# Kernel optimization log

Hardware: AMD Instinct MI355X
Metric: run time of the kernel (lower is better)

Reference implementation:

```python
import jax, jax.numpy as jnp
import numpy as np
import math

HIDDEN = 2048
N_HEADS = 32
N_KV_HEADS = 8
HEAD_DIM = HIDDEN // N_HEADS  # 64
N_REP = N_HEADS // N_KV_HEADS  # 4
ROPE_THETA = 10000.0
BSZ, SEQ = 2, 2048


def setup_inputs() -> dict:
    key = jax.random.key(0)
    ks = jax.random.split(key, 6)
    hidden_states = jax.random.normal(ks[0], (BSZ, SEQ, HIDDEN), dtype=jnp.float32)
    wq = jax.random.normal(ks[1], (HIDDEN, N_HEADS * HEAD_DIM), dtype=jnp.float32) * (HIDDEN ** -0.5)
    wk = jax.random.normal(ks[2], (HIDDEN, N_KV_HEADS * HEAD_DIM), dtype=jnp.float32) * (HIDDEN ** -0.5)
    wv = jax.random.normal(ks[3], (HIDDEN, N_KV_HEADS * HEAD_DIM), dtype=jnp.float32) * (HIDDEN ** -0.5)
    wo = jax.random.normal(ks[4], (N_HEADS * HEAD_DIM, HIDDEN), dtype=jnp.float32) * (HIDDEN ** -0.5)
    # additive causal mask [b, 1, q, kv]
    neg = jnp.finfo(jnp.float32).min
    causal = jnp.where(jnp.tril(jnp.ones((SEQ, SEQ), dtype=bool)), 0.0, neg)
    attention_mask = jnp.broadcast_to(causal[None, None], (BSZ, 1, SEQ, SEQ)).astype(jnp.float32)
    position_ids = jnp.broadcast_to(jnp.arange(SEQ, dtype=jnp.int32)[None], (BSZ, SEQ))
    return {
        "hidden_states": hidden_states,
        "wq": wq, "wk": wk, "wv": wv, "wo": wo,
        "attention_mask": attention_mask,
        "position_ids": position_ids,
    }


def _rope_cache(seq_len, dtype):
    inv_freq = 1.0 / (ROPE_THETA ** (jnp.arange(0, HEAD_DIM, 2, dtype=jnp.float32) / HEAD_DIM))
    t = jnp.arange(seq_len, dtype=jnp.float32)
    freqs = jnp.outer(t, inv_freq)              # [S, head_dim/2]
    emb = jnp.concatenate([freqs, freqs], -1)   # [S, head_dim]
    return jnp.cos(emb).astype(dtype), jnp.sin(emb).astype(dtype)


def _rotate_half(x):
    x1, x2 = jnp.split(x, 2, axis=-1)
    return jnp.concatenate([-x2, x1], axis=-1)


def reference(hidden_states, wq, wk, wv, wo, attention_mask, position_ids):
    b, s, _ = hidden_states.shape
    q = (hidden_states @ wq).reshape(b, s, N_HEADS, HEAD_DIM).transpose(0, 2, 1, 3)
    k = (hidden_states @ wk).reshape(b, s, N_KV_HEADS, HEAD_DIM).transpose(0, 2, 1, 3)
    v = (hidden_states @ wv).reshape(b, s, N_KV_HEADS, HEAD_DIM).transpose(0, 2, 1, 3)

    cos_c, sin_c = _rope_cache(s, hidden_states.dtype)
    cos = cos_c[position_ids][:, None]  # [b,1,s,head_dim]
    sin = sin_c[position_ids][:, None]
    q = q * cos + _rotate_half(q) * sin
    k = k * cos + _rotate_half(k) * sin

    # repeat_kv: [b, kvh, s, d] -> [b, kvh*n_rep, s, d]
    k = jnp.broadcast_to(k[:, :, None], (b, N_KV_HEADS, N_REP, s, HEAD_DIM)).reshape(b, N_HEADS, s, HEAD_DIM)
    v = jnp.broadcast_to(v[:, :, None], (b, N_KV_HEADS, N_REP, s, HEAD_DIM)).reshape(b, N_HEADS, s, HEAD_DIM)

    scores = jnp.einsum('bhqd,bhkd->bhqk', q, k) / math.sqrt(HEAD_DIM)
    scores = scores + attention_mask
    probs = jax.nn.softmax(scores.astype(jnp.float32), axis=-1).astype(q.dtype)
    attn = jnp.einsum('bhqk,bhkd->bhqd', probs, v)  # [b,h,s,d]
    attn = attn.transpose(0, 2, 1, 3).reshape(b, s, N_HEADS * HEAD_DIM)
    return attn @ wo
```

## Files before the change

kernel.cpp:

```cpp
#include <hip/hip_runtime.h>
#include <math.h>


typedef float f32x4 __attribute__((ext_vector_type(4)));
typedef short s16x8 __attribute__((ext_vector_type(8)));
typedef unsigned short u16x4 __attribute__((ext_vector_type(4)));

__device__ __forceinline__ unsigned short f2bf(float x) {
    union { float f; unsigned int u; } v; v.f = x;
    unsigned int r = v.u + 0x7FFF + ((v.u >> 16) & 1);
    return (unsigned short)(r >> 16);
}

__global__ __launch_bounds__(256) void cast_f32_bf16(
    const float* __restrict__ in, unsigned short* __restrict__ out) {
    size_t i = (size_t)blockIdx.x * 256 + threadIdx.x;
    f32x4 v = *(const f32x4*)&in[i * 4];
    u16x4 r;
    r[0] = f2bf(v[0]); r[1] = f2bf(v[1]); r[2] = f2bf(v[2]); r[3] = f2bf(v[3]);
    *(u16x4*)&out[i * 4] = r;
}

__global__ __launch_bounds__(256) void transpose_cast_all(
    const float* __restrict__ Wq, const float* __restrict__ Wk,
    const float* __restrict__ Wv, const float* __restrict__ Wo,
    unsigned short* __restrict__ Wqkvt, unsigned short* __restrict__ Wot) {
    __shared__ float t[32][33];
    const int bx = blockIdx.x;
    const float* W; unsigned short* Out; int N, n0, nb;
    if (bx < 64)      { W = Wq; Out = Wqkvt; N = 2048; n0 = 0;    nb = bx; }
    else if (bx < 80) { W = Wk; Out = Wqkvt; N = 512;  n0 = 2048; nb = bx - 64; }
    else if (bx < 96) { W = Wv; Out = Wqkvt; N = 512;  n0 = 2560; nb = bx - 80; }
    else              { W = Wo; Out = Wot;   N = 2048; n0 = 0;    nb = bx - 96; }
    int kb = blockIdx.y * 32; nb *= 32;
    int tx = threadIdx.x & 31, ty = threadIdx.x >> 5;
#pragma unroll
    for (int i = 0; i < 4; ++i)
        t[ty + i * 8][tx] = W[(size_t)(kb + ty + i * 8) * N + nb + tx];
    __syncthreads();
#pragma unroll
    for (int i = 0; i < 4; ++i)
        Out[(size_t)(n0 + nb + ty + i * 8) * 2048 + kb + tx] = f2bf(t[tx][ty + i * 8]);
}

__global__ __launch_bounds__(256) void gemm_qkv_rope(
    const unsigned short* __restrict__ A, const unsigned short* __restrict__ Bt,
    const int* __restrict__ pos,
    unsigned short* __restrict__ Qb, unsigned short* __restrict__ Kb,
    unsigned short* __restrict__ Vb) {
    const int K = 2048;
    __shared__ unsigned short As[128 * 64];
    __shared__ unsigned short Bs[128 * 64];
    const int tid = threadIdx.x;
    const int wave = tid >> 6, lane = tid & 63;
    const int col = lane & 15, quad = lane >> 4;
    const int m0 = blockIdx.y * 128, n0 = blockIdx.x * 128;
    const int wm = (wave >> 1) * 64, wn = (wave & 1) * 64;

    const int lrow = lane >> 3;
    const int gch = (lane & 7) ^ lrow;
    const unsigned short* Ag = A + (size_t)(m0 + wave * 32 + lrow) * K + gch * 8;
    const unsigned short* Bg = Bt + (size_t)(n0 + wave * 32 + lrow) * K + gch * 8;
    unsigned short* AsW = As + wave * 2048;
    unsigned short* BsW = Bs + wave * 2048;

    f32x4 acc[4][4] = {};

    for (int k0 = 0; k0 < K; k0 += 64) {
#pragma unroll
        for (int i = 0; i < 4; ++i) {
            __builtin_amdgcn_global_load_lds(
                (const __attribute__((address_space(1))) void*)(Ag + (size_t)i * 8 * K + k0),
                (__attribute__((address_space(3))) void*)(AsW + i * 512), 16, 0, 0);
            __builtin_amdgcn_global_load_lds(
                (const __attribute__((address_space(1))) void*)(Bg + (size_t)i * 8 * K + k0),
                (__attribute__((address_space(3))) void*)(BsW + i * 512), 16, 0, 0);
        }
        __syncthreads();
#pragma unroll
        for (int ks = 0; ks < 2; ++ks) {
            const int slot = ((ks << 2) + quad) ^ (col & 7);
            s16x8 af[4], bf[4];
#pragma unroll
            for (int mi = 0; mi < 4; ++mi)
                af[mi] = *(const s16x8*)&As[(wm + mi * 16 + col) * 64 + slot * 8];
#pragma unroll
            for (int ni = 0; ni < 4; ++ni)
                bf[ni] = *(const s16x8*)&Bs[(wn + ni * 16 + col) * 64 + slot * 8];
#pragma unroll
            for (int mi = 0; mi < 4; ++mi)
#pragma unroll
                for (int ni = 0; ni < 4; ++ni)
                    acc[mi][ni] = __builtin_amdgcn_mfma_f32_16x16x32_bf16(
                        af[mi], bf[ni], acc[mi][ni], 0, 0, 0);
        }
        __syncthreads();
    }

    const int cb = n0 + wn;
    if (cb >= 2560) {
        const int hd = (cb - 2560) >> 6;
#pragma unroll
        for (int mi = 0; mi < 4; ++mi)
#pragma unroll
            for (int r = 0; r < 4; ++r) {
                int m = m0 + wm + mi * 16 + quad * 4 + r;
                int b = m >> 11, s = m & 2047;
                size_t rb = ((size_t)(b * 8 + hd) * 2048 + s) * 64;
#pragma unroll
                for (int ni = 0; ni < 4; ++ni)
                    Vb[rb + ni * 16 + col] = f2bf(acc[mi][ni][r]);
            }
    } else {
        const int isQ = (cb < 2048);
        const int hd = isQ ? (cb >> 6) : ((cb - 2048) >> 6);
        const int nh = isQ ? 32 : 8;
        const float scale = isQ ? 0.125f : 1.0f;
        unsigned short* Out = isQ ? Qb : Kb;
        const float NEG_LN_TH_32 = -0.28782313662425575f;
        const float inv0 = __expf((float)col * NEG_LN_TH_32);
        const float inv1 = __expf((float)(col + 16) * NEG_LN_TH_32);
#pragma unroll
        for (int mi = 0; mi < 4; ++mi)
#pragma unroll
            for (int r = 0; r < 4; ++r) {
                int m = m0 + wm + mi * 16 + quad * 4 + r;
                int b = m >> 11, s = m & 2047;
                float p = (float)pos[m];
                float sn0, cs0, sn1, cs1;
                __sincosf(p * inv0, &sn0, &cs0);
                __sincosf(p * inv1, &sn1, &cs1);
                float a0 = acc[mi][0][r], a1 = acc[mi][1][r];
                float b0 = acc[mi][2][r], b1 = acc[mi][3][r];
                size_t rb = ((size_t)(b * nh + hd) * 2048 + s) * 64;
                Out[rb + col]      = f2bf((a0 * cs0 - b0 * sn0) * scale);
                Out[rb + col + 16] = f2bf((a1 * cs1 - b1 * sn1) * scale);
                Out[rb + col + 32] = f2bf((b0 * cs0 + a0 * sn0) * scale);
                Out[rb + col + 48] = f2bf((b1 * cs1 + a1 * sn1) * scale);
            }
    }
}

__global__ __launch_bounds__(256) void gemm_bf16_nt(
    const unsigned short* __restrict__ A, const unsigned short* __restrict__ Bt,
    float* __restrict__ C, int K, int ldc) {
    __shared__ unsigned short As[128 * 64];
    __shared__ unsigned short Bs[128 * 64];
    const int tid = threadIdx.x;
    const int wave = tid >> 6, lane = tid & 63;
    const int col = lane & 15, quad = lane >> 4;
    const int m0 = blockIdx.y * 128, n0 = blockIdx.x * 128;
    const int wm = (wave >> 1) * 64, wn = (wave & 1) * 64;

    const int lrow = lane >> 3;
    const int gch = (lane & 7) ^ lrow;
    const unsigned short* Ag = A + (size_t)(m0 + wave * 32 + lrow) * K + gch * 8;
    const unsigned short* Bg = Bt + (size_t)(n0 + wave * 32 + lrow) * K + gch * 8;
    unsigned short* AsW = As + wave * 2048;
    unsigned short* BsW = Bs + wave * 2048;

    f32x4 acc[4][4] = {};

    for (int k0 = 0; k0 < K; k0 += 64) {
#pragma unroll
        for (int i = 0; i < 4; ++i) {
            __builtin_amdgcn_global_load_lds(
                (const __attribute__((address_space(1))) void*)(Ag + (size_t)i * 8 * K + k0),
                (__attribute__((address_space(3))) void*)(AsW + i * 512), 16, 0, 0);
            __builtin_amdgcn_global_load_lds(
                (const __attribute__((address_space(1))) void*)(Bg + (size_t)i * 8 * K + k0),
                (__attribute__((address_space(3))) void*)(BsW + i * 512), 16, 0, 0);
        }
        __syncthreads();
#pragma unroll
        for (int ks = 0; ks < 2; ++ks) {
            const int slot = ((ks << 2) + quad) ^ (col & 7);
            s16x8 af[4], bf[4];
#pragma unroll
            for (int mi = 0; mi < 4; ++mi)
                af[mi] = *(const s16x8*)&As[(wm + mi * 16 + col) * 64 + slot * 8];
#pragma unroll
            for (int ni = 0; ni < 4; ++ni)
                bf[ni] = *(const s16x8*)&Bs[(wn + ni * 16 + col) * 64 + slot * 8];
#pragma unroll
            for (int mi = 0; mi < 4; ++mi)
#pragma unroll
                for (int ni = 0; ni < 4; ++ni)
                    acc[mi][ni] = __builtin_amdgcn_mfma_f32_16x16x32_bf16(
                        af[mi], bf[ni], acc[mi][ni], 0, 0, 0);
        }
        __syncthreads();
    }
#pragma unroll
    for (int mi = 0; mi < 4; ++mi)
#pragma unroll
        for (int ni = 0; ni < 4; ++ni)
#pragma unroll
            for (int r = 0; r < 4; ++r) {
                int m = m0 + wm + mi * 16 + quad * 4 + r;
                int n = n0 + wn + ni * 16 + col;
                C[(size_t)m * ldc + n] = acc[mi][ni][r];
            }
}

__global__ __launch_bounds__(256) void transpose_v(
    const unsigned short* __restrict__ Vb, unsigned short* __restrict__ Vt) {
    __shared__ unsigned short t[64 * 66];
    const int bh = blockIdx.x >> 5, st = blockIdx.x & 31;
    const unsigned short* src = Vb + ((size_t)bh * 2048 + st * 64) * 64;
    unsigned short* dst = Vt + (size_t)bh * 64 * 2048 + st * 64;
    const int r = threadIdx.x >> 2, c = (threadIdx.x & 3) * 16;
    s16x8 v0 = *(const s16x8*)&src[r * 64 + c];
    s16x8 v1 = *(const s16x8*)&src[r * 64 + c + 8];
    unsigned* tw = (unsigned*)&t[r * 66 + c];
#pragma unroll
    for (int q2 = 0; q2 < 4; ++q2) tw[q2] = ((unsigned*)&v0)[q2];
#pragma unroll
    for (int q2 = 0; q2 < 4; ++q2) tw[4 + q2] = ((unsigned*)&v1)[q2];
    __syncthreads();
    const int d = threadIdx.x >> 2, sc2 = (threadIdx.x & 3) * 16;
    unsigned short outv[16];
#pragma unroll
    for (int jj = 0; jj < 16; ++jj) outv[jj] = t[(sc2 + jj) * 66 + d];
    *(s16x8*)&dst[(size_t)d * 2048 + sc2] = *(s16x8*)&outv[0];
    *(s16x8*)&dst[(size_t)d * 2048 + sc2 + 8] = *(s16x8*)&outv[8];
}

__global__ __launch_bounds__(256, 4) void flash_attn(
    const unsigned short* __restrict__ Qb, const unsigned short* __restrict__ Kb,
    const unsigned short* __restrict__ Vt, unsigned short* __restrict__ Ob) {
    __shared__ unsigned short Ks[64 * 64];
    __shared__ unsigned short Vs[64 * 64];
    __shared__ unsigned short PsA[4][16 * 64];
    __shared__ unsigned short PsB[4][16 * 64];

    const int tid = threadIdx.x;
    const int wave = tid >> 6, lane = tid & 63;
    const int col = lane & 15, quad = lane >> 4;

    const int id = blockIdx.x;
    const int j = id & 15, bh = id >> 4;
    const int b = bh >> 5, h = bh & 31, kvh = h >> 2;
    const int qA0 = (31 - j) * 64, qB0 = j * 64;
    const int qwA = qA0 + wave * 16, qwB = qB0 + wave * 16;

    const unsigned short* Qg  = Qb + ((size_t)(b * 32 + h) * 2048) * 64;
    const unsigned short* Kgb = Kb + ((size_t)(b * 8 + kvh) * 2048) * 64;
    const unsigned short* Vgb = Vt + ((size_t)(b * 8 + kvh) * 64) * 2048;

    const int r8 = lane >> 3, g = (lane & 7) ^ r8;
    const unsigned short* KgL = Kgb + (size_t)(wave * 16 + r8) * 64 + g * 8;
    const unsigned short* VgL = Vgb + (size_t)(wave * 16 + r8) * 2048 + g * 8;
    unsigned short* KsW = Ks + wave * 16 * 64;
    unsigned short* VsW = Vs + wave * 16 * 64;

    const s16x8 onesf = {16256, 16256, 16256, 16256, 16256, 16256, 16256, 16256};

    s16x8 qfA[2], qfB[2];
#pragma unroll
    for (int ks = 0; ks < 2; ++ks) {
        qfA[ks] = *(const s16x8*)&Qg[(size_t)(qwA + col) * 64 + ks * 32 + quad * 8];
        qfB[ks] = *(const s16x8*)&Qg[(size_t)(qwB + col) * 64 + ks * 32 + quad * 8];
    }

    f32x4 aoA[4] = {}, aoB[4] = {};
    f32x4 alA = {}, alB = {};

    for (int kv0 = 0; kv0 <= qA0; kv0 += 64) {
        __builtin_amdgcn_global_load_lds(
            (const __attribute__((address_space(1))) void*)(KgL + (size_t)kv0 * 64),
            (__attribute__((address_space(3))) void*)KsW, 16, 0, 0);
        __builtin_amdgcn_global_load_lds(
            (const __attribute__((address_space(1))) void*)(KgL + (size_t)kv0 * 64 + 512),
            (__attribute__((address_space(3))) void*)(KsW + 512), 16, 0, 0);
        __builtin_amdgcn_global_load_lds(
            (const __attribute__((address_space(1))) void*)(VgL + kv0),
            (__attribute__((address_space(3))) void*)VsW, 16, 0, 0);
        __builtin_amdgcn_global_load_lds(
            (const __attribute__((address_space(1))) void*)(VgL + kv0 + 8 * 2048),
            (__attribute__((address_space(3))) void*)(VsW + 512), 16, 0, 0);
        __syncthreads();

        const bool doB = (kv0 <= qB0);
#pragma unroll
        for (int mi = 0; mi < 4; ++mi) {
            const int s0 = (quad) ^ (col & 7);
            const int s1 = (4 + quad) ^ (col & 7);
            s16x8 kf0 = *(const s16x8*)&Ks[(mi * 16 + col) * 64 + s0 * 8];
            s16x8 kf1 = *(const s16x8*)&Ks[(mi * 16 + col) * 64 + s1 * 8];
            {
                f32x4 sc = {};
                sc = __builtin_amdgcn_mfma_f32_16x16x32_bf16(kf0, qfA[0], sc, 0, 0, 0);
                sc = __builtin_amdgcn_mfma_f32_16x16x32_bf16(kf1, qfA[1], sc, 0, 0, 0);
                if (kv0 == qA0) {
                    int kvb = kv0 + mi * 16 + quad * 4, q = qwA + col;
#pragma unroll
                    for (int r = 0; r < 4; ++r)
                        if (kvb + r > q) sc[r] = -1e30f;
                }
                unsigned eb[4];
#pragma unroll
                for (int r = 0; r < 4; ++r) eb[r] = __float_as_uint(__expf(sc[r]));
                uint2 pk;
                pk.x = __builtin_amdgcn_perm(eb[1], eb[0], 0x07060302u);
                pk.y = __builtin_amdgcn_perm(eb[3], eb[2], 0x07060302u);
                int chl = (mi * 2 + (quad >> 1)) ^ (col & 7);
                *(uint2*)&PsA[wave][col * 64 + chl * 8 + (quad & 1) * 4] = pk;
            }
            if (doB) {
                f32x4 sc = {};
                sc = __builtin_amdgcn_mfma_f32_16x16x32_bf16(kf0, qfB[0], sc, 0, 0, 0);
                sc = __builtin_amdgcn_mfma_f32_16x16x32_bf16(kf1, qfB[1], sc, 0, 0, 0);
                if (kv0 == qB0) {
                    int kvb = kv0 + mi * 16 + quad * 4, q = qwB + col;
#pragma unroll
                    for (int r = 0; r < 4; ++r)
                        if (kvb + r > q) sc[r] = -1e30f;
                }
                unsigned eb[4];
#pragma unroll
                for (int r = 0; r < 4; ++r) eb[r] = __float_as_uint(__expf(sc[r]));
                uint2 pk;
                pk.x = __builtin_amdgcn_perm(eb[1], eb[0], 0x07060302u);
                pk.y = __builtin_amdgcn_perm(eb[3], eb[2], 0x07060302u);
                int chl = (mi * 2 + (quad >> 1)) ^ (col & 7);
                *(uint2*)&PsB[wave][col * 64 + chl * 8 + (quad & 1) * 4] = pk;
            }
        }
        asm volatile("s_waitcnt lgkmcnt(0)" ::: "memory");
#pragma unroll
        for (int ks = 0; ks < 2; ++ks) {
            const int slot = ((ks << 2) + quad) ^ (col & 7);
            s16x8 vf[4];
#pragma unroll
            for (int di = 0; di < 4; ++di)
                vf[di] = *(const s16x8*)&Vs[(di * 16 + col) * 64 + slot * 8];
            s16x8 pfA = *(const s16x8*)&PsA[wave][col * 64 + slot * 8];
            alA = __builtin_amdgcn_mfma_f32_16x16x32_bf16(pfA, onesf, alA, 0, 0, 0);
#pragma unroll
            for (int di = 0; di < 4; ++di)
                aoA[di] = __builtin_amdgcn_mfma_f32_16x16x32_bf16(pfA, vf[di], aoA[di], 0, 0, 0);
            if (doB) {
                s16x8 pfB = *(const s16x8*)&PsB[wave][col * 64 + slot * 8];
                alB = __builtin_amdgcn_mfma_f32_16x16x32_bf16(pfB, onesf, alB, 0, 0, 0);
#pragma unroll
                for (int di = 0; di < 4; ++di)
                    aoB[di] = __builtin_amdgcn_mfma_f32_16x16x32_bf16(pfB, vf[di], aoB[di], 0, 0, 0);
            }
        }
        __syncthreads();
    }

#pragma unroll
    for (int r = 0; r < 4; ++r) {
        {
            int qg = qwA + quad * 4 + r;
            float inv = 1.f / alA[r];
            size_t base = ((size_t)b * 2048 + qg) * 2048 + h * 64;
#pragma unroll
            for (int di = 0; di < 4; ++di)
                Ob[base + di * 16 + col] = f2bf(aoA[di][r] * inv);
        }
        {
            int qg = qwB + quad * 4 + r;
            float inv = 1.f / alB[r];
            size_t base = ((size_t)b * 2048 + qg) * 2048 + h * 64;
#pragma unroll
            for (int di = 0; di < 4; ++di)
                Ob[base + di * 16 + col] = f2bf(aoB[di][r] * inv);
        }
    }
}

extern "C" void kernel_launch(void* const* d_in, const int* in_sizes, int n_in,
                              void* d_out, int out_size, void* d_ws, size_t ws_size,
                              hipStream_t stream) {
    const float* X  = (const float*)d_in[0];
    const float* Wq = (const float*)d_in[1];
    const float* Wk = (const float*)d_in[2];
    const float* Wv = (const float*)d_in[3];
    const float* Wo = (const float*)d_in[4];
    const int* pos  = (const int*)d_in[6];
    float* out = (float*)d_out;

    char* ws = (char*)d_ws;
    unsigned short* Xb    = (unsigned short*)(ws + 0);
    unsigned short* Wqkvt = (unsigned short*)(ws + 16777216);
    unsigned short* Wot   = (unsigned short*)(ws + 29360128);
    unsigned short* Qb    = (unsigned short*)(ws + 37748736);
    unsigned short* Kb    = (unsigned short*)(ws + 54525952);
    unsigned short* Vb    = (unsigned short*)(ws + 58720256);
    unsigned short* Vt    = (unsigned short*)(ws + 62914560);
    unsigned short* Attn  = Xb;

    cast_f32_bf16<<<8192, 256, 0, stream>>>(X, Xb);
    transpose_cast_all<<<dim3(160, 64), 256, 0, stream>>>(Wq, Wk, Wv, Wo, Wqkvt, Wot);
    gemm_qkv_rope<<<dim3(24, 32), 256, 0, stream>>>(Xb, Wqkvt, pos, Qb, Kb, Vb);
    transpose_v<<<512, 256, 0, stream>>>(Vb, Vt);
    flash_attn<<<1024, 256, 0, stream>>>(Qb, Kb, Vt, Attn);
    gemm_bf16_nt<<<dim3(16, 32), 256, 0, stream>>>(Attn, Wot, out, 2048, 2048);
}
```

Measured before the change: 316.9 us.

## Use two waves per attention block with 32 query rows each; fuse prep kernels

Flash attention now runs 128-thread blocks where each wave handles two 16-row query chunks, so every K/V fragment read from LDS is reused across 32 query rows and each wave issues more of the global-to-LDS copies. Block-to-tile assignment is also rotated by bh group to spread causal work across CUs. The X cast and the weight transpose-cast kernels are merged into one launch to save a launch. The cost is higher register pressure from doubled accumulators and fewer waves per block to hide latency.

```diff
diff --git a/kernel.cpp b/kernel.cpp
--- a/kernel.cpp
+++ b/kernel.cpp
@@ -12,27 +12,30 @@
     return (unsigned short)(r >> 16);
 }
 
-__global__ __launch_bounds__(256) void cast_f32_bf16(
-    const float* __restrict__ in, unsigned short* __restrict__ out) {
-    size_t i = (size_t)blockIdx.x * 256 + threadIdx.x;
-    f32x4 v = *(const f32x4*)&in[i * 4];
-    u16x4 r;
-    r[0] = f2bf(v[0]); r[1] = f2bf(v[1]); r[2] = f2bf(v[2]); r[3] = f2bf(v[3]);
-    *(u16x4*)&out[i * 4] = r;
-}
-
-__global__ __launch_bounds__(256) void transpose_cast_all(
-    const float* __restrict__ Wq, const float* __restrict__ Wk,
-    const float* __restrict__ Wv, const float* __restrict__ Wo,
-    unsigned short* __restrict__ Wqkvt, unsigned short* __restrict__ Wot) {
+__global__ __launch_bounds__(256) void prep(
+    const float* __restrict__ X, const float* __restrict__ Wq,
+    const float* __restrict__ Wk, const float* __restrict__ Wv,
+    const float* __restrict__ Wo,
+    unsigned short* __restrict__ Xb, unsigned short* __restrict__ Wqkvt,
+    unsigned short* __restrict__ Wot) {
+    const int bid = blockIdx.x;
+    if (bid < 8192) {
+        size_t i = (size_t)bid * 256 + threadIdx.x;
+        f32x4 v = *(const f32x4*)&X[i * 4];
+        u16x4 r;
+        r[0] = f2bf(v[0]); r[1] = f2bf(v[1]); r[2] = f2bf(v[2]); r[3] = f2bf(v[3]);
+        *(u16x4*)&Xb[i * 4] = r;
+        return;
+    }
     __shared__ float t[32][33];
-    const int bx = blockIdx.x;
+    const int tb = bid - 8192;
+    const int kbi = tb / 160, bx = tb - kbi * 160;
     const float* W; unsigned short* Out; int N, n0, nb;
     if (bx < 64)      { W = Wq; Out = Wqkvt; N = 2048; n0 = 0;    nb = bx; }
     else if (bx < 80) { W = Wk; Out = Wqkvt; N = 512;  n0 = 2048; nb = bx - 64; }
     else if (bx < 96) { W = Wv; Out = Wqkvt; N = 512;  n0 = 2560; nb = bx - 80; }
     else              { W = Wo; Out = Wot;   N = 2048; n0 = 0;    nb = bx - 96; }
-    int kb = blockIdx.y * 32; nb *= 32;
+    int kb = kbi * 32; nb *= 32;
     int tx = threadIdx.x & 31, ty = threadIdx.x >> 5;
 #pragma unroll
     for (int i = 0; i < 4; ++i)
@@ -226,74 +229,75 @@
     *(s16x8*)&dst[(size_t)d * 2048 + sc2 + 8] = *(s16x8*)&outv[8];
 }
 
-__global__ __launch_bounds__(256, 4) void flash_attn(
+__global__ __launch_bounds__(128, 2) void flash_attn(
     const unsigned short* __restrict__ Qb, const unsigned short* __restrict__ Kb,
     const unsigned short* __restrict__ Vt, unsigned short* __restrict__ Ob) {
     __shared__ unsigned short Ks[64 * 64];
     __shared__ unsigned short Vs[64 * 64];
-    __shared__ unsigned short PsA[4][16 * 64];
-    __shared__ unsigned short PsB[4][16 * 64];
+    __shared__ unsigned short PsA[2][32 * 64];
+    __shared__ unsigned short PsB[2][32 * 64];
 
     const int tid = threadIdx.x;
     const int wave = tid >> 6, lane = tid & 63;
     const int col = lane & 15, quad = lane >> 4;
 
     const int id = blockIdx.x;
-    const int j = id & 15, bh = id >> 4;
+    const int j = ((id & 15) + ((id >> 8) << 2)) & 15;
+    const int bh = id >> 4;
     const int b = bh >> 5, h = bh & 31, kvh = h >> 2;
     const int qA0 = (31 - j) * 64, qB0 = j * 64;
-    const int qwA = qA0 + wave * 16, qwB = qB0 + wave * 16;
+    const int qwA = qA0 + wave * 32, qwB = qB0 + wave * 32;
 
     const unsigned short* Qg  = Qb + ((size_t)(b * 32 + h) * 2048) * 64;
     const unsigned short* Kgb = Kb + ((size_t)(b * 8 + kvh) * 2048) * 64;
     const unsigned short* Vgb = Vt + ((size_t)(b * 8 + kvh) * 64) * 2048;
 
     const int r8 = lane >> 3, g = (lane & 7) ^ r8;
-    const unsigned short* KgL = Kgb + (size_t)(wave * 16 + r8) * 64 + g * 8;
-    const unsigned short* VgL = Vgb + (size_t)(wave * 16 + r8) * 2048 + g * 8;
-    unsigned short* KsW = Ks + wave * 16 * 64;
-    unsigned short* VsW = Vs + wave * 16 * 64;
+    const unsigned short* KgL = Kgb + (size_t)(wave * 32 + r8) * 64 + g * 8;
+    const unsigned short* VgL = Vgb + (size_t)(wave * 32 + r8) * 2048 + g * 8;
+    unsigned short* KsW = Ks + wave * 32 * 64;
+    unsigned short* VsW = Vs + wave * 32 * 64;
 
     const s16x8 onesf = {16256, 16256, 16256, 16256, 16256, 16256, 16256, 16256};
 
-    s16x8 qfA[2], qfB[2];
-#pragma unroll
-    for (int ks = 0; ks < 2; ++ks) {
-        qfA[ks] = *(const s16x8*)&Qg[(size_t)(qwA + col) * 64 + ks * 32 + quad * 8];
-        qfB[ks] = *(const s16x8*)&Qg[(size_t)(qwB + col) * 64 + ks * 32 + quad * 8];
-    }
-
-    f32x4 aoA[4] = {}, aoB[4] = {};
-    f32x4 alA = {}, alB = {};
+    s16x8 qfA[2][2], qfB[2][2];
+#pragma unroll
+    for (int qc = 0; qc < 2; ++qc)
+#pragma unroll
+        for (int ks = 0; ks < 2; ++ks) {
+            qfA[qc][ks] = *(const s16x8*)&Qg[(size_t)(qwA + qc * 16 + col) * 64 + ks * 32 + quad * 8];
+            qfB[qc][ks] = *(const s16x8*)&Qg[(size_t)(qwB + qc * 16 + col) * 64 + ks * 32 + quad * 8];
+        }
+
+    f32x4 aoA[2][4] = {}, aoB[2][4] = {};
+    f32x4 alA[2] = {}, alB[2] = {};
 
     for (int kv0 = 0; kv0 <= qA0; kv0 += 64) {
-        __builtin_amdgcn_global_load_lds(
-            (const __attribute__((address_space(1))) void*)(KgL + (size_t)kv0 * 64),
-            (__attribute__((address_space(3))) void*)KsW, 16, 0, 0);
-        __builtin_amdgcn_global_load_lds(
-            (const __attribute__((address_space(1))) void*)(KgL + (size_t)kv0 * 64 + 512),
-            (__attribute__((address_space(3))) void*)(KsW + 512), 16, 0, 0);
-        __builtin_amdgcn_global_load_lds(
-            (const __attribute__((address_space(1))) void*)(VgL + kv0),
-            (__attribute__((address_space(3))) void*)VsW, 16, 0, 0);
-        __builtin_amdgcn_global_load_lds(
-            (const __attribute__((address_space(1))) void*)(VgL + kv0 + 8 * 2048),
-            (__attribute__((address_space(3))) void*)(VsW + 512), 16, 0, 0);
-        __syncthreads();
-
+#pragma unroll
+        for (int i = 0; i < 4; ++i) {
+            __builtin_amdgcn_global_load_lds(
+                (const __attribute__((address_space(1))) void*)(KgL + (size_t)(kv0 + i * 8) * 64),
+                (__attribute__((address_space(3))) void*)(KsW + i * 512), 16, 0, 0);
+            __builtin_amdgcn_global_load_lds(
+                (const __attribute__((address_space(1))) void*)(VgL + kv0 + (size_t)i * 8 * 2048),
+                (__attribute__((address_space(3))) void*)(VsW + i * 512), 16, 0, 0);
+        }
+        __syncthreads();
         const bool doB = (kv0 <= qB0);
 #pragma unroll
         for (int mi = 0; mi < 4; ++mi) {
-            const int s0 = (quad) ^ (col & 7);
+            const int s0 = quad ^ (col & 7);
             const int s1 = (4 + quad) ^ (col & 7);
             s16x8 kf0 = *(const s16x8*)&Ks[(mi * 16 + col) * 64 + s0 * 8];
             s16x8 kf1 = *(const s16x8*)&Ks[(mi * 16 + col) * 64 + s1 * 8];
-            {
+            const int chl = (mi * 2 + (quad >> 1)) ^ (col & 7);
+#pragma unroll
+            for (int qc = 0; qc < 2; ++qc) {
                 f32x4 sc = {};
-                sc = __builtin_amdgcn_mfma_f32_16x16x32_bf16(kf0, qfA[0], sc, 0, 0, 0);
-                sc = __builtin_amdgcn_mfma_f32_16x16x32_bf16(kf1, qfA[1], sc, 0, 0, 0);
+                sc = __builtin_amdgcn_mfma_f32_16x16x32_bf16(kf0, qfA[qc][0], sc, 0, 0, 0);
+                sc = __builtin_amdgcn_mfma_f32_16x16x32_bf16(kf1, qfA[qc][1], sc, 0, 0, 0);
                 if (kv0 == qA0) {
-                    int kvb = kv0 + mi * 16 + quad * 4, q = qwA + col;
+                    int kvb = kv0 + mi * 16 + quad * 4, q = qwA + qc * 16 + col;
 #pragma unroll
                     for (int r = 0; r < 4; ++r)
                         if (kvb + r > q) sc[r] = -1e30f;
@@ -304,27 +308,28 @@
                 uint2 pk;
                 pk.x = __builtin_amdgcn_perm(eb[1], eb[0], 0x07060302u);
                 pk.y = __builtin_amdgcn_perm(eb[3], eb[2], 0x07060302u);
-                int chl = (mi * 2 + (quad >> 1)) ^ (col & 7);
-                *(uint2*)&PsA[wave][col * 64 + chl * 8 + (quad & 1) * 4] = pk;
+                *(uint2*)&PsA[wave][(qc * 16 + col) * 64 + chl * 8 + (quad & 1) * 4] = pk;
             }
             if (doB) {
-                f32x4 sc = {};
-                sc = __builtin_amdgcn_mfma_f32_16x16x32_bf16(kf0, qfB[0], sc, 0, 0, 0);
-                sc = __builtin_amdgcn_mfma_f32_16x16x32_bf16(kf1, qfB[1], sc, 0, 0, 0);
-                if (kv0 == qB0) {
-                    int kvb = kv0 + mi * 16 + quad * 4, q = qwB + col;
-#pragma unroll
-                    for (int r = 0; r < 4; ++r)
-                        if (kvb + r > q) sc[r] = -1e30f;
+#pragma unroll
+                for (int qc = 0; qc < 2; ++qc) {
+                    f32x4 sc = {};
+                    sc = __builtin_amdgcn_mfma_f32_16x16x32_bf16(kf0, qfB[qc][0], sc, 0, 0, 0);
+                    sc = __builtin_amdgcn_mfma_f32_16x16x32_bf16(kf1, qfB[qc][1], sc, 0, 0, 0);
+                    if (kv0 == qB0) {
+                        int kvb = kv0 + mi * 16 + quad * 4, q = qwB + qc * 16 + col;
+#pragma unroll
+                        for (int r = 0; r < 4; ++r)
+                            if (kvb + r > q) sc[r] = -1e30f;
+                    }
+                    unsigned eb[4];
+#pragma unroll
+                    for (int r = 0; r < 4; ++r) eb[r] = __float_as_uint(__expf(sc[r]));
+                    uint2 pk;
+                    pk.x = __builtin_amdgcn_perm(eb[1], eb[0], 0x07060302u);
+                    pk.y = __builtin_amdgcn_perm(eb[3], eb[2], 0x07060302u);
+                    *(uint2*)&PsB[wave][(qc * 16 + col) * 64 + chl * 8 + (quad & 1) * 4] = pk;
                 }
-                unsigned eb[4];
-#pragma unroll
-                for (int r = 0; r < 4; ++r) eb[r] = __float_as_uint(__expf(sc[r]));
-                uint2 pk;
-                pk.x = __builtin_amdgcn_perm(eb[1], eb[0], 0x07060302u);
-                pk.y = __builtin_amdgcn_perm(eb[3], eb[2], 0x07060302u);
-                int chl = (mi * 2 + (quad >> 1)) ^ (col & 7);
-                *(uint2*)&PsB[wave][col * 64 + chl * 8 + (quad & 1) * 4] = pk;
             }
         }
         asm volatile("s_waitcnt lgkmcnt(0)" ::: "memory");
@@ -335,41 +340,49 @@
 #pragma unroll
             for (int di = 0; di < 4; ++di)
                 vf[di] = *(const s16x8*)&Vs[(di * 16 + col) * 64 + slot * 8];
-            s16x8 pfA = *(const s16x8*)&PsA[wave][col * 64 + slot * 8];
-            alA = __builtin_amdgcn_mfma_f32_16x16x32_bf16(pfA, onesf, alA, 0, 0, 0);
-#pragma unroll
-            for (int di = 0; di < 4; ++di)
-                aoA[di] = __builtin_amdgcn_mfma_f32_16x16x32_bf16(pfA, vf[di], aoA[di], 0, 0, 0);
+#pragma unroll
+            for (int qc = 0; qc < 2; ++qc) {
+                s16x8 pfA = *(const s16x8*)&PsA[wave][(qc * 16 + col) * 64 + slot * 8];
+                alA[qc] = __builtin_amdgcn_mfma_f32_16x16x32_bf16(pfA, onesf, alA[qc], 0, 0, 0);
+#pragma unroll
+                for (int di = 0; di < 4; ++di)
+                    aoA[qc][di] = __builtin_amdgcn_mfma_f32_16x16x32_bf16(pfA, vf[di], aoA[qc][di], 0, 0, 0);
+            }
             if (doB) {
-                s16x8 pfB = *(const s16x8*)&PsB[wave][col * 64 + slot * 8];
-                alB = __builtin_amdgcn_mfma_f32_16x16x32_bf16(pfB, onesf, alB, 0, 0, 0);
+#pragma unroll
+                for (int qc = 0; qc < 2; ++qc) {
+                    s16x8 pfB = *(const s16x8*)&PsB[wave][(qc * 16 + col) * 64 + slot * 8];
+                    alB[qc] = __builtin_amdgcn_mfma_f32_16x16x32_bf16(pfB, onesf, alB[qc], 0, 0, 0);
+#pragma unroll
+                    for (int di = 0; di < 4; ++di)
+                        aoB[qc][di] = __builtin_amdgcn_mfma_f32_16x16x32_bf16(pfB, vf[di], aoB[qc][di], 0, 0, 0);
+                }
+            }
+        }
+        __syncthreads();
+    }
+
+#pragma unroll
+    for (int qc = 0; qc < 2; ++qc)
+#pragma unroll
+        for (int r = 0; r < 4; ++r) {
+            {
+                int qg = qwA + qc * 16 + quad * 4 + r;
+                float inv = 1.f / alA[qc][r];
+                size_t base = ((size_t)b * 2048 + qg) * 2048 + h * 64;
 #pragma unroll
                 for (int di = 0; di < 4; ++di)
-                    aoB[di] = __builtin_amdgcn_mfma_f32_16x16x32_bf16(pfB, vf[di], aoB[di], 0, 0, 0);
-            }
-        }
-        __syncthreads();
-    }
-
-#pragma unroll
-    for (int r = 0; r < 4; ++r) {
-        {
-            int qg = qwA + quad * 4 + r;
-            float inv = 1.f / alA[r];
-            size_t base = ((size_t)b * 2048 + qg) * 2048 + h * 64;
-#pragma unroll
-            for (int di = 0; di < 4; ++di)
-                Ob[base + di * 16 + col] = f2bf(aoA[di][r] * inv);
-        }
-        {
-            int qg = qwB + quad * 4 + r;
-            float inv = 1.f / alB[r];
-            size_t base = ((size_t)b * 2048 + qg) * 2048 + h * 64;
-#pragma unroll
-            for (int di = 0; di < 4; ++di)
-                Ob[base + di * 16 + col] = f2bf(aoB[di][r] * inv);
-        }
-    }
+                    Ob[base + di * 16 + col] = f2bf(aoA[qc][di][r] * inv);
+            }
+            {
+                int qg = qwB + qc * 16 + quad * 4 + r;
+                float inv = 1.f / alB[qc][r];
+                size_t base = ((size_t)b * 2048 + qg) * 2048 + h * 64;
+#pragma unroll
+                for (int di = 0; di < 4; ++di)
+                    Ob[base + di * 16 + col] = f2bf(aoB[qc][di][r] * inv);
+            }
+        }
 }
 
 extern "C" void kernel_launch(void* const* d_in, const int* in_sizes, int n_in,
@@ -393,10 +406,9 @@
     unsigned short* Vt    = (unsigned short*)(ws + 62914560);
     unsigned short* Attn  = Xb;
 
-    cast_f32_bf16<<<8192, 256, 0, stream>>>(X, Xb);
-    transpose_cast_all<<<dim3(160, 64), 256, 0, stream>>>(Wq, Wk, Wv, Wo, Wqkvt, Wot);
+    prep<<<18432, 256, 0, stream>>>(X, Wq, Wk, Wv, Wo, Xb, Wqkvt, Wot);
     gemm_qkv_rope<<<dim3(24, 32), 256, 0, stream>>>(Xb, Wqkvt, pos, Qb, Kb, Vb);
     transpose_v<<<512, 256, 0, stream>>>(Vb, Vt);
-    flash_attn<<<1024, 256, 0, stream>>>(Qb, Kb, Vt, Attn);
+    flash_attn<<<1024, 128, 0, stream>>>(Qb, Kb, Vt, Attn);
     gemm_bf16_nt<<<dim3(16, 32), 256, 0, stream>>>(Attn, Wot, out, 2048, 2048);
 }
```

After: 315.9 us. No clear change (-0.3%).
